# Kernel tuning notes

Hardware: AMD Instinct MI355X
Metric: run time of the kernel (lower is better)

Reference implementation:

```python
import jax, jax.numpy as jnp
import numpy as np

B, N, EPG = 64, 512, 8192
E = B * EPG
K1 = int(np.ceil(0.8 * N))    # 410
K2 = int(np.ceil(0.8 * K1))   # 328


def setup_inputs() -> dict:
    key = jax.random.key(0)
    ks = jax.random.split(key, 32)
    x = jax.random.normal(ks[0], (B * N, 32), jnp.float32)
    edge_attr = jax.random.normal(ks[1], (E, 100), jnp.float32)
    src_l = jax.random.randint(ks[2], (E,), 0, N)
    dst_l = jax.random.randint(ks[3], (E,), 0, N)
    off = jnp.repeat(jnp.arange(B, dtype=jnp.int64) * N, EPG)
    edge_index = jnp.stack([src_l + off, dst_l + off]).astype(jnp.int64)
    batch = jnp.repeat(jnp.arange(B, dtype=jnp.int64), N)

    def lin(k, fin, fout):
        s = 1.0 / np.sqrt(fin)
        k1, k2 = jax.random.split(k)
        return (jax.random.uniform(k1, (fin, fout), jnp.float32, -s, s),
                jax.random.uniform(k2, (fout,), jnp.float32, -s, s))

    dec1_w, dec1_b = lin(ks[4], 100, 64)
    dec2_w, dec2_b = lin(ks[5], 64, 32)
    mlp1_w, mlp1_b = lin(ks[6], 32, 128)
    mlp2_w, mlp2_b = lin(ks[7], 128, 256)
    pool1_w = jax.random.normal(ks[8], (256,), jnp.float32) * 0.1
    gat_w = jax.random.normal(ks[9], (256, 256), jnp.float32) * (1.0 / np.sqrt(256))
    gat_att_src = jax.random.normal(ks[10], (4, 64), jnp.float32) * 0.1
    gat_att_dst = jax.random.normal(ks[11], (4, 64), jnp.float32) * 0.1
    gat_b = jnp.zeros((256,), jnp.float32)
    pool2_w = jax.random.normal(ks[12], (256,), jnp.float32) * 0.1
    lin1_w, lin1_b = lin(ks[13], 512, 128)
    lin2_w, lin2_b = lin(ks[14], 128, 64)
    lin3_w, lin3_b = lin(ks[15], 64, 2)
    return dict(x=x, edge_index=edge_index, batch=batch, edge_attr=edge_attr,
                dec1_w=dec1_w, dec1_b=dec1_b, dec2_w=dec2_w, dec2_b=dec2_b,
                mlp1_w=mlp1_w, mlp1_b=mlp1_b, mlp2_w=mlp2_w, mlp2_b=mlp2_b,
                pool1_w=pool1_w, gat_w=gat_w, gat_att_src=gat_att_src,
                gat_att_dst=gat_att_dst, gat_b=gat_b, pool2_w=pool2_w,
                lin1_w=lin1_w, lin1_b=lin1_b, lin2_w=lin2_w, lin2_b=lin2_b,
                lin3_w=lin3_w, lin3_b=lin3_b)


def _forward(x, edge_attr, dec1_w, dec1_b, dec2_w, dec2_b, mlp1_w, mlp1_b,
             mlp2_w, mlp2_b, pool1_w, gat_w, gat_att_src, gat_att_dst, gat_b,
             pool2_w, lin1_w, lin1_b, lin2_w, lin2_b, lin3_w, lin3_b,
             src, dst):
    # edge encoder
    ea = jax.nn.relu(edge_attr @ dec1_w + dec1_b)
    ea = jax.nn.relu(ea @ dec2_w + dec2_b)                       # [E,32]
    # GINEConv (eps=0): sum_j relu(x_j + e_ji), then mlp((1+eps)x + aggr)
    msg = jax.nn.relu(x[src] + ea)
    agg = jax.ops.segment_sum(msg, dst, num_segments=B * N)
    h = x + agg
    h = jax.nn.relu(h @ mlp1_w + mlp1_b) @ mlp2_w + mlp2_b       # [BN,256]
    h = jax.nn.relu(h)
    # TopKPooling 1 (uniform graphs -> fixed k)
    s = jnp.tanh((h @ pool1_w) / jnp.linalg.norm(pool1_w))       # [BN]
    topv, topi = jax.lax.top_k(s.reshape(B, N), K1)              # [B,K1]
    gperm = (topi + jnp.arange(B)[:, None] * N).reshape(-1)
    hp = h[gperm] * topv.reshape(-1)[:, None]                    # [B*K1,256]
    kept = jnp.zeros(B * N, bool).at[gperm].set(True)
    newid = jnp.zeros(B * N, jnp.int32).at[gperm].set(jnp.arange(B * K1, dtype=jnp.int32))
    src1, dst1 = newid[src], newid[dst]
    valid = kept[src] & kept[dst]
    # readout 1: global max + mean pool
    hr = hp.reshape(B, K1, 256)
    x1 = jnp.concatenate([hr.max(axis=1), hr.mean(axis=1)], axis=-1)  # [B,512]
    # GATConv(256, 64, heads=4) with self-loops; invalid edges masked
    Nk = B * K1
    loops = jnp.arange(Nk, dtype=jnp.int32)
    src2 = jnp.concatenate([src1, loops])
    dst2 = jnp.concatenate([dst1, loops])
    valid2 = jnp.concatenate([valid, jnp.ones(Nk, bool)])
    xl = (hp @ gat_w).reshape(Nk, 4, 64)
    a_src = (xl * gat_att_src).sum(-1)                           # [Nk,4]
    a_dst = (xl * gat_att_dst).sum(-1)
    logit = jax.nn.leaky_relu(a_src[src2] + a_dst[dst2], 0.2)    # [E2,4]
    logit = jnp.where(valid2[:, None], logit, -jnp.inf)
    m = jax.ops.segment_max(logit, dst2, num_segments=Nk)
    e = jnp.where(valid2[:, None], jnp.exp(logit - m[dst2]), 0.0)
    den = jax.ops.segment_sum(e, dst2, num_segments=Nk)
    alpha = e / den[dst2]
    out = jax.ops.segment_sum(alpha[:, :, None] * xl[src2], dst2, num_segments=Nk)
    g = jax.nn.relu(out.reshape(Nk, 256) + gat_b)
    # TopKPooling 2 (pooled edges unused downstream)
    s2 = jnp.tanh((g @ pool2_w) / jnp.linalg.norm(pool2_w))
    topv2, topi2 = jax.lax.top_k(s2.reshape(B, K1), K2)
    gperm2 = (topi2 + jnp.arange(B)[:, None] * K1).reshape(-1)
    gp = (g[gperm2] * topv2.reshape(-1)[:, None]).reshape(B, K2, 256)
    x2 = jnp.concatenate([gp.max(axis=1), gp.mean(axis=1)], axis=-1)
    # head (dropout = identity in eval)
    z = x1 + x2
    z = jax.nn.relu(z @ lin1_w + lin1_b)
    z = jax.nn.relu(z @ lin2_w + lin2_b)
    return jax.nn.log_softmax(z @ lin3_w + lin3_b, axis=-1)     # [B,2]


def reference(x, edge_index, batch, edge_attr, dec1_w, dec1_b, dec2_w, dec2_b,
              mlp1_w, mlp1_b, mlp2_w, mlp2_b, pool1_w, gat_w, gat_att_src,
              gat_att_dst, gat_b, pool2_w, lin1_w, lin1_b, lin2_w, lin2_b,
              lin3_w, lin3_b):
    src = edge_index[0].astype(jnp.int32)
    dst = edge_index[1].astype(jnp.int32)
    return _forward(x, edge_attr, dec1_w, dec1_b, dec2_w, dec2_b, mlp1_w,
                    mlp1_b, mlp2_w, mlp2_b, pool1_w, gat_w, gat_att_src,
                    gat_att_dst, gat_b, pool2_w, lin1_w, lin1_b, lin2_w,
                    lin2_b, lin3_w, lin3_b, src, dst)
```

## Files before the change

### kernel.cpp

```cpp
#include <hip/hip_runtime.h>
#include <math.h>

#define B_   64
#define N_   512
#define E_   524288
#define BN_  32768
#define K1_  410
#define K2_  328
#define NK_  26240
#define KC_  25

__device__ __forceinline__ float lrelu(float x) { return x > 0.f ? x : 0.2f * x; }

__global__ __launch_bounds__(256) void norm_kernel(const float* __restrict__ p1,
                                                   const float* __restrict__ p2,
                                                   float* __restrict__ norms) {
    __shared__ float r1[256], r2[256];
    int t = threadIdx.x;
    float a = p1[t], b = p2[t];
    r1[t] = a * a; r2[t] = b * b;
    for (int o = 128; o > 0; o >>= 1) {
        __syncthreads();
        if (t < o) { r1[t] += r1[t + o]; r2[t] += r2[t + o]; }
    }
    __syncthreads();
    if (t == 0) { norms[0] = sqrtf(r1[0]); norms[1] = sqrtf(r2[0]); }
}

template <int NSEG>
__global__ __launch_bounds__(1024) void scan_kernel(int* __restrict__ cnt, int* __restrict__ offsets)
{
    __shared__ int part[1024];
    int t = threadIdx.x;
    const int CH = (NSEG + 1023) / 1024;
    int base = t * CH;
    int sum = 0;
    for (int i = 0; i < CH; ++i) { int gi = base + i; if (gi < NSEG) sum += cnt[gi]; }
    part[t] = sum;
    __syncthreads();
    for (int o = 1; o < 1024; o <<= 1) {
        int v = (t >= o) ? part[t - o] : 0;
        __syncthreads();
        part[t] += v;
        __syncthreads();
    }
    int run = (t == 0) ? 0 : part[t - 1];
    for (int i = 0; i < CH; ++i) {
        int gi = base + i;
        if (gi < NSEG) { offsets[gi] = run; run += cnt[gi]; cnt[gi] = 0; }
    }
    if (t == 1023) offsets[NSEG] = part[1023];
}

__global__ __launch_bounds__(256) void count_node_kernel(const int* __restrict__ dstG,
                                                         int* __restrict__ cnt_node)
{
    int e = blockIdx.x * blockDim.x + threadIdx.x;
    atomicAdd(&cnt_node[dstG[e]], 1);
}

__global__ __launch_bounds__(256) void fill_node_kernel(const int* __restrict__ dstG,
                                                        const int* __restrict__ offs_node,
                                                        int* __restrict__ cnt_node,
                                                        int* __restrict__ pos_e)
{
    int e = blockIdx.x * blockDim.x + threadIdx.x;
    int d = dstG[e];
    int p = offs_node[d] + atomicAdd(&cnt_node[d], 1);
    pos_e[e] = p;
}

__global__ __launch_bounds__(256) void edge_mlp_kernel(
    const float* __restrict__ edge_attr, const int* __restrict__ srcG,
    const int* __restrict__ pos_e,
    const float* __restrict__ x,
    const float* __restrict__ W1, const float* __restrict__ b1,
    const float* __restrict__ W2, const float* __restrict__ b2,
    float* __restrict__ msg_sorted)
{
    __shared__ float bufAT[KC_][68];
    __shared__ float w1cT[KC_][64];
    __shared__ float ea1T[64][68];
    __shared__ float w2s[64][32];
    __shared__ float b2s[32];
    __shared__ int   srcs[64], poss[64];

    int tid = threadIdx.x;
    int eb  = blockIdx.x * 64;

    if (tid < 64) { srcs[tid] = srcG[eb + tid]; poss[tid] = pos_e[eb + tid]; }
    for (int i = tid; i < 64 * 32; i += 256) w2s[i >> 5][i & 31] = W2[i];
    if (tid >= 192 && tid < 224) b2s[tid - 192] = b2[tid - 192];

    int tx = tid & 15, ty = tid >> 4;
    float b1v[4];
#pragma unroll
    for (int j = 0; j < 4; ++j) b1v[j] = b1[tx * 4 + j];

    float acc[4][4] = {};

    float raA[7], raB[7], rw[7];
    auto issueA = [&](int kc, float (&ra)[7]) {
#pragma unroll
        for (int u = 0; u < 7; ++u) {
            int i = tid + u * 256;
            if (i < 1600) {
                int e = i / 25, k = i - e * 25;
                ra[u] = edge_attr[(size_t)(eb + e) * 100 + kc + k];
            }
        }
    };
    auto issueW = [&](int kc) {
#pragma unroll
        for (int u = 0; u < 7; ++u) {
            int i = tid + u * 256;
            if (i < 1600) rw[u] = W1[(size_t)(kc + (i >> 6)) * 64 + (i & 63)];
        }
    };
    auto lwriteA = [&](float (&ra)[7]) {
#pragma unroll
        for (int u = 0; u < 7; ++u) {
            int i = tid + u * 256;
            if (i < 1600) {
                int e = i / 25, k = i - e * 25;
                bufAT[k][e] = ra[u];
            }
        }
    };
    auto lwriteW = [&]() {
#pragma unroll
        for (int u = 0; u < 7; ++u) {
            int i = tid + u * 256;
            if (i < 1600) w1cT[i >> 6][i & 63] = rw[u];
        }
    };

    issueA(0, raA);
    issueW(0);
    issueA(KC_, raB);
    lwriteA(raA); lwriteW();
    __syncthreads();

#pragma unroll
    for (int c = 0; c < 4; ++c) {
        if (c == 0) issueA(2 * KC_, raA);
        if (c == 1) issueA(3 * KC_, raB);
        if (c < 3)  issueW((c + 1) * KC_);
#pragma unroll 5
        for (int k = 0; k < KC_; ++k) {
            float4 a4 = *(const float4*)&bufAT[k][ty * 4];
            float4 w4 = *(const float4*)&w1cT[k][tx * 4];
            float a[4] = { a4.x, a4.y, a4.z, a4.w };
            float w[4] = { w4.x, w4.y, w4.z, w4.w };
#pragma unroll
            for (int i = 0; i < 4; ++i)
#pragma unroll
                for (int j = 0; j < 4; ++j) acc[i][j] += a[i] * w[j];
        }
        if (c < 3) {
            __syncthreads();
            if ((c & 1) == 0) lwriteA(raB);
            else              lwriteA(raA);
            lwriteW();
            __syncthreads();
        }
    }
#pragma unroll
    for (int j = 0; j < 4; ++j) {
        float4 v;
        v.x = fmaxf(acc[0][j] + b1v[j], 0.f);
        v.y = fmaxf(acc[1][j] + b1v[j], 0.f);
        v.z = fmaxf(acc[2][j] + b1v[j], 0.f);
        v.w = fmaxf(acc[3][j] + b1v[j], 0.f);
        *(float4*)&ea1T[tx * 4 + j][ty * 4] = v;
    }
    __syncthreads();

    int e0 = (tid >> 3) * 2;
    int c0 = (tid & 7) * 4;
    float acc2[2][4] = {};
    for (int k = 0; k < 64; ++k) {
        float2 a2 = *(const float2*)&ea1T[k][e0];
        float4 w4 = *(const float4*)&w2s[k][c0];
        float w[4] = { w4.x, w4.y, w4.z, w4.w };
#pragma unroll
        for (int j = 0; j < 4; ++j) {
            acc2[0][j] += a2.x * w[j]; acc2[1][j] += a2.y * w[j];
        }
    }
#pragma unroll
    for (int r = 0; r < 2; ++r) {
        int e = e0 + r, s = srcs[e];
        const float4 xv = *(const float4*)(x + (size_t)s * 32 + c0);
        float xa[4] = { xv.x, xv.y, xv.z, xv.w };
        float4 m;
        m.x = fmaxf(xa[0] + fmaxf(acc2[r][0] + b2s[c0 + 0], 0.f), 0.f);
        m.y = fmaxf(xa[1] + fmaxf(acc2[r][1] + b2s[c0 + 1], 0.f), 0.f);
        m.z = fmaxf(xa[2] + fmaxf(acc2[r][2] + b2s[c0 + 2], 0.f), 0.f);
        m.w = fmaxf(xa[3] + fmaxf(acc2[r][3] + b2s[c0 + 3], 0.f), 0.f);
        *(float4*)(msg_sorted + (size_t)poss[e] * 32 + c0) = m;
    }
}

__global__ __launch_bounds__(256) void segsum_kernel(const float* __restrict__ msg_sorted,
                                                     const int* __restrict__ offs_n,
                                                     float* __restrict__ agg)
{
    int wid  = (blockIdx.x * blockDim.x + threadIdx.x) >> 6;
    int lane = threadIdx.x & 63;
    if (wid >= BN_) return;
    int off0 = offs_n[wid], off1 = offs_n[wid + 1];
    int col = lane & 31, rr = lane >> 5;
    float sum = 0.f;
    for (int j = off0 + rr; j < off1; j += 2)
        sum += msg_sorted[(size_t)j * 32 + col];
    sum += __shfl_xor(sum, 32);
    if (lane < 32) agg[(size_t)wid * 32 + col] = sum;
}

template <int ACT, bool HASBIAS, bool HASA2, bool GATHER>
__global__ __launch_bounds__(256) void gemm_tile128(
    const float* __restrict__ A, const float* __restrict__ A2,
    const int* __restrict__ rowidx, const float* __restrict__ rowscale,
    const float* __restrict__ W, const float* __restrict__ bias,
    float* __restrict__ C, int M, int N, int K)
{
    __shared__ float As[16][132];
    __shared__ float Ws[16][132];
    int tid = threadIdx.x;
    int tx = tid & 15, ty = tid >> 4;
    int mb = blockIdx.y * 128, nb = blockIdx.x * 128;
    float acc[8][8] = {};

    int am = tid & 127;
    int ak = (tid >> 7) * 8;
    int wk = tid >> 4;
    int wn = (tid & 15) * 8;

    int   arow  = mb + am;
    float ascal = 1.f;
    if (GATHER) { ascal = rowscale[arow]; arow = rowidx[arow]; }

    for (int kt = 0; kt < K; kt += 16) {
        {
            const float* pa = A + (size_t)arow * K + kt + ak;
            float4 v0 = *(const float4*)(pa);
            float4 v1 = *(const float4*)(pa + 4);
            if (HASA2) {
                const float* pb = A2 + (size_t)arow * K + kt + ak;
                float4 u0 = *(const float4*)(pb);
                float4 u1 = *(const float4*)(pb + 4);
                v0.x += u0.x; v0.y += u0.y; v0.z += u0.z; v0.w += u0.w;
                v1.x += u1.x; v1.y += u1.y; v1.z += u1.z; v1.w += u1.w;
            }
            if (GATHER) {
                v0.x *= ascal; v0.y *= ascal; v0.z *= ascal; v0.w *= ascal;
                v1.x *= ascal; v1.y *= ascal; v1.z *= ascal; v1.w *= ascal;
            }
            As[ak + 0][am] = v0.x; As[ak + 1][am] = v0.y;
            As[ak + 2][am] = v0.z; As[ak + 3][am] = v0.w;
            As[ak + 4][am] = v1.x; As[ak + 5][am] = v1.y;
            As[ak + 6][am] = v1.z; As[ak + 7][am] = v1.w;
        }
        {
            const float* pw = W + (size_t)(kt + wk) * N + nb + wn;
            *(float4*)&Ws[wk][wn]     = *(const float4*)(pw);
            *(float4*)&Ws[wk][wn + 4] = *(const float4*)(pw + 4);
        }
        __syncthreads();
#pragma unroll
        for (int k2 = 0; k2 < 16; ++k2) {
            float4 a0 = *(const float4*)&As[k2][ty * 8];
            float4 a1 = *(const float4*)&As[k2][ty * 8 + 4];
            float4 w0 = *(const float4*)&Ws[k2][tx * 4];
            float4 w1 = *(const float4*)&Ws[k2][64 + tx * 4];
            float a[8] = { a0.x, a0.y, a0.z, a0.w, a1.x, a1.y, a1.z, a1.w };
            float w[8] = { w0.x, w0.y, w0.z, w0.w, w1.x, w1.y, w1.z, w1.w };
#pragma unroll
            for (int i = 0; i < 8; ++i)
#pragma unroll
                for (int j = 0; j < 8; ++j) acc[i][j] += a[i] * w[j];
        }
        __syncthreads();
    }
#pragma unroll
    for (int i = 0; i < 8; ++i) {
        int m = mb + ty * 8 + i;
        int col0 = nb + tx * 4, col1 = nb + 64 + tx * 4;
        float r[8];
#pragma unroll
        for (int j = 0; j < 4; ++j) {
            float v = acc[i][j];
            if (HASBIAS) v += bias[col0 + j];
            if (ACT == 1) v = fmaxf(v, 0.f);
            r[j] = v;
        }
#pragma unroll
        for (int j = 4; j < 8; ++j) {
            float v = acc[i][j];
            if (HASBIAS) v += bias[col1 + j - 4];
            if (ACT == 1) v = fmaxf(v, 0.f);
            r[j] = v;
        }
        float4 o0 = { r[0], r[1], r[2], r[3] };
        float4 o1 = { r[4], r[5], r[6], r[7] };
        *(float4*)&C[(size_t)m * N + col0] = o0;
        *(float4*)&C[(size_t)m * N + col1] = o1;
    }
}

__global__ __launch_bounds__(256) void scores_kernel(const float* __restrict__ P,
                                                     const float* __restrict__ w,
                                                     const float* __restrict__ norms, int nidx,
                                                     float* __restrict__ s, int R)
{
    int wid  = (blockIdx.x * blockDim.x + threadIdx.x) >> 6;
    int lane = threadIdx.x & 63;
    if (wid >= R) return;
    float acc = 0.f;
#pragma unroll
    for (int r = 0; r < 4; ++r) {
        int d = r * 64 + lane;
        acc += P[(size_t)wid * 256 + d] * w[d];
    }
    for (int o = 32; o > 0; o >>= 1) acc += __shfl_xor(acc, o);
    if (lane == 0) s[wid] = tanhf(acc / norms[nidx]);
}

__device__ void bitonic_desc512(float* val, int* idx, int t) {
    for (int k = 2; k <= 512; k <<= 1) {
        for (int j = k >> 1; j > 0; j >>= 1) {
            __syncthreads();
            int ixj = t ^ j;
            if (ixj > t) {
                float v0 = val[t], v1 = val[ixj];
                int   i0 = idx[t], i1 = idx[ixj];
                bool before = (v0 > v1) || (v0 == v1 && i0 < i1);
                bool dir = ((t & k) == 0);
                bool doswap = dir ? (!before) : before;
                if (doswap) { val[t] = v1; val[ixj] = v0; idx[t] = i1; idx[ixj] = i0; }
            }
        }
    }
    __syncthreads();
}

__global__ __launch_bounds__(512) void topk1_kernel(const float* __restrict__ s,
                                                    float* __restrict__ topval,
                                                    int* __restrict__ topnode,
                                                    int* __restrict__ kept,
                                                    int* __restrict__ newid)
{
    __shared__ float val[512];
    __shared__ int   idx[512];
    int b = blockIdx.x, t = threadIdx.x;
    val[t] = s[b * N_ + t]; idx[t] = t;
    bitonic_desc512(val, idx, t);
    if (t < K1_) {
        int node = b * N_ + idx[t];
        int orow = b * K1_ + t;
        topnode[orow] = node;
        topval[orow]  = val[t];
        kept[node]  = 1;
        newid[node] = orow;
    }
}

__global__ __launch_bounds__(1024) void readout1_kernel(const float* __restrict__ h,
                                                        const int* __restrict__ topnode,
                                                        const float* __restrict__ topval,
                                                        float* __restrict__ zbuf)
{
    __shared__ float rmx[1024], rsm[1024];
    int b = blockIdx.x >> 2, cg = blockIdx.x & 3;
    int tid = threadIdx.x;
    int cl = tid & 63, rg = tid >> 6;
    int c = cg * 64 + cl;
    float mx = -INFINITY, sm = 0.f;
    for (int j = rg; j < K1_; j += 16) {
        int row = topnode[b * K1_ + j];
        float v = h[(size_t)row * 256 + c] * topval[b * K1_ + j];
        mx = fmaxf(mx, v); sm += v;
    }
    rmx[tid] = mx; rsm[tid] = sm;
    __syncthreads();
    if (tid < 512) { rmx[tid] = fmaxf(rmx[tid], rmx[tid + 512]); rsm[tid] += rsm[tid + 512]; }
    __syncthreads();
    if (tid < 256) { rmx[tid] = fmaxf(rmx[tid], rmx[tid + 256]); rsm[tid] += rsm[tid + 256]; }
    __syncthreads();
    if (tid < 128) { rmx[tid] = fmaxf(rmx[tid], rmx[tid + 128]); rsm[tid] += rsm[tid + 128]; }
    __syncthreads();
    if (tid < 64) {
        zbuf[b * 512 + c]       = fmaxf(rmx[tid], rmx[tid + 64]);
        zbuf[b * 512 + 256 + c] = (rsm[tid] + rsm[tid + 64]) / (float)K1_;
    }
}

__global__ __launch_bounds__(256) void attcoef_kernel(const float* __restrict__ xl,
                                                      const float* __restrict__ att_src,
                                                      const float* __restrict__ att_dst,
                                                      float* __restrict__ a_src,
                                                      float* __restrict__ a_dst)
{
    int wid  = (blockIdx.x * blockDim.x + threadIdx.x) >> 6;
    int lane = threadIdx.x & 63;
    if (wid >= NK_) return;
    float vs[4], vd[4];
#pragma unroll
    for (int r = 0; r < 4; ++r) {
        int d = r * 64 + lane;
        float v = xl[(size_t)wid * 256 + d];
        vs[r] = v * att_src[d];
        vd[r] = v * att_dst[d];
    }
    for (int o = 32; o > 0; o >>= 1) {
#pragma unroll
        for (int r = 0; r < 4; ++r) {
            vs[r] += __shfl_xor(vs[r], o);
            vd[r] += __shfl_xor(vd[r], o);
        }
    }
    if (lane == 0) {
#pragma unroll
        for (int r = 0; r < 4; ++r) {
            a_src[wid * 4 + r] = vs[r];
            a_dst[wid * 4 + r] = vd[r];
        }
    }
}

__global__ __launch_bounds__(256) void count_kernel(const int* __restrict__ srcG,
                                                    const int* __restrict__ dstG,
                                                    const int* __restrict__ kept,
                                                    const int* __restrict__ newid,
                                                    int* __restrict__ cnt)
{
    int e = blockIdx.x * blockDim.x + threadIdx.x;
    int s = srcG[e], d = dstG[e];
    if (kept[s] && kept[d]) atomicAdd(&cnt[newid[d]], 1);
}

__global__ __launch_bounds__(256) void fill_kernel(const int* __restrict__ srcG,
                                                   const int* __restrict__ dstG,
                                                   const int* __restrict__ kept,
                                                   const int* __restrict__ newid,
                                                   const int* __restrict__ offsets,
                                                   int* __restrict__ cnt,
                                                   int* __restrict__ csr_src)
{
    int e = blockIdx.x * blockDim.x + threadIdx.x;
    int s = srcG[e], d = dstG[e];
    if (kept[s] && kept[d]) {
        int d1 = newid[d];
        int p = offsets[d1] + atomicAdd(&cnt[d1], 1);
        csr_src[p] = newid[s];
    }
}

__global__ __launch_bounds__(256) void gat_agg_kernel(const float* __restrict__ xl,
                                                      const float* __restrict__ a_src,
                                                      const float* __restrict__ a_dst,
                                                      const int* __restrict__ offsets,
                                                      const int* __restrict__ csr_src,
                                                      const float* __restrict__ gat_b,
                                                      const float* __restrict__ pool2_w,
                                                      const float* __restrict__ norms,
                                                      float* __restrict__ g,
                                                      float* __restrict__ s2)
{
    int wid  = (blockIdx.x * blockDim.x + threadIdx.x) >> 6;
    int lane = threadIdx.x & 63;
    if (wid >= NK_) return;
    int off0 = offsets[wid], off1 = offsets[wid + 1];

    float4 ad = *(const float4*)(a_dst + (size_t)wid * 4);
    float4 asf = *(const float4*)(a_src + (size_t)wid * 4);
    float adv[4] = { ad.x, ad.y, ad.z, ad.w };
    float lsf[4] = { lrelu(asf.x + ad.x), lrelu(asf.y + ad.y),
                     lrelu(asf.z + ad.z), lrelu(asf.w + ad.w) };

    float den[4] = {};
    float acc[4] = {};
    int e = off0;
    for (; e + 1 < off1; e += 2) {
        int s1 = csr_src[e], s2v = csr_src[e + 1];
        float4 a1 = *(const float4*)(a_src + (size_t)s1 * 4);
        float4 a2 = *(const float4*)(a_src + (size_t)s2v * 4);
        float av1[4] = { a1.x, a1.y, a1.z, a1.w };
        float av2[4] = { a2.x, a2.y, a2.z, a2.w };
#pragma unroll
        for (int r = 0; r < 4; ++r) {
            float w1 = expf(fminf(lrelu(av1[r] + adv[r]), 80.f));
            float w2 = expf(fminf(lrelu(av2[r] + adv[r]), 80.f));
            float x1 = xl[(size_t)s1 * 256 + r * 64 + lane];
            float x2 = xl[(size_t)s2v * 256 + r * 64 + lane];
            den[r] += w1 + w2;
            acc[r] += w1 * x1 + w2 * x2;
        }
    }
    if (e < off1) {
        int s1 = csr_src[e];
        float4 a1 = *(const float4*)(a_src + (size_t)s1 * 4);
        float av1[4] = { a1.x, a1.y, a1.z, a1.w };
#pragma unroll
        for (int r = 0; r < 4; ++r) {
            float w1 = expf(fminf(lrelu(av1[r] + adv[r]), 80.f));
            den[r] += w1;
            acc[r] += w1 * xl[(size_t)s1 * 256 + r * 64 + lane];
        }
    }
    float gv[4];
#pragma unroll
    for (int r = 0; r < 4; ++r) {
        float ws = expf(fminf(lsf[r], 80.f));
        den[r] += ws;
        acc[r] = (acc[r] + ws * xl[(size_t)wid * 256 + r * 64 + lane]) / den[r];
        int d = r * 64 + lane;
        gv[r] = fmaxf(acc[r] + gat_b[d], 0.f);
        g[(size_t)wid * 256 + d] = gv[r];
    }
    float dot = 0.f;
#pragma unroll
    for (int r = 0; r < 4; ++r) dot += gv[r] * pool2_w[r * 64 + lane];
    for (int o = 32; o > 0; o >>= 1) dot += __shfl_xor(dot, o);
    if (lane == 0) s2[wid] = tanhf(dot / norms[1]);
}

__global__ __launch_bounds__(512) void topk2_sort_kernel(const float* __restrict__ s2,
                                                         int* __restrict__ t2row,
                                                         float* __restrict__ t2val)
{
    __shared__ float val[512];
    __shared__ int   idx[512];
    int b = blockIdx.x, t = threadIdx.x;
    val[t] = (t < K1_) ? s2[b * K1_ + t] : -INFINITY;
    idx[t] = t;
    bitonic_desc512(val, idx, t);
    if (t < K2_) {
        t2row[b * K2_ + t] = b * K1_ + idx[t];
        t2val[b * K2_ + t] = val[t];
    }
}

__global__ __launch_bounds__(512) void readout2_kernel(const float* __restrict__ g,
                                                       const int* __restrict__ t2row,
                                                       const float* __restrict__ t2val,
                                                       float* __restrict__ zbuf)
{
    __shared__ float rmx[512], rsm[512];
    int b = blockIdx.x >> 2, cg = blockIdx.x & 3;
    int tid = threadIdx.x;
    int cl = tid & 63, rg = tid >> 6;
    int c = cg * 64 + cl;
    float mx = -INFINITY, sm = 0.f;
    for (int j = rg; j < K2_; j += 8) {
        int row = t2row[b * K2_ + j];
        float v = g[(size_t)row * 256 + c] * t2val[b * K2_ + j];
        mx = fmaxf(mx, v); sm += v;
    }
    rmx[tid] = mx; rsm[tid] = sm;
    __syncthreads();
    if (tid < 256) { rmx[tid] = fmaxf(rmx[tid], rmx[tid + 256]); rsm[tid] += rsm[tid + 256]; }
    __syncthreads();
    if (tid < 128) { rmx[tid] = fmaxf(rmx[tid], rmx[tid + 128]); rsm[tid] += rsm[tid + 128]; }
    __syncthreads();
    if (tid < 64) {
        zbuf[b * 512 + c]       += fmaxf(rmx[tid], rmx[tid + 64]);
        zbuf[b * 512 + 256 + c] += (rsm[tid] + rsm[tid + 64]) / (float)K2_;
    }
}

__global__ __launch_bounds__(128) void head_kernel(const float* __restrict__ zbuf,
                                                   const float* __restrict__ l1w, const float* __restrict__ l1b,
                                                   const float* __restrict__ l2w, const float* __restrict__ l2b,
                                                   const float* __restrict__ l3w, const float* __restrict__ l3b,
                                                   float* __restrict__ out)
{
    __shared__ float zs[512];
    __shared__ float h1s[128];
    __shared__ float h2s[64];
    __shared__ float os[2];
    int b = blockIdx.x, t = threadIdx.x;
    for (int i = t; i < 512; i += 128) zs[i] = zbuf[b * 512 + i];
    __syncthreads();
    float acc = l1b[t];
    for (int k = 0; k < 512; ++k) acc += zs[k] * l1w[k * 128 + t];
    h1s[t] = fmaxf(acc, 0.f);
    __syncthreads();
    if (t < 64) {
        float a2 = l2b[t];
        for (int k = 0; k < 128; ++k) a2 += h1s[k] * l2w[k * 64 + t];
        h2s[t] = fmaxf(a2, 0.f);
    }
    __syncthreads();
    if (t < 2) {
        float a3 = l3b[t];
        for (int k = 0; k < 64; ++k) a3 += h2s[k] * l3w[k * 2 + t];
        os[t] = a3;
    }
    __syncthreads();
    if (t == 0) {
        float m = fmaxf(os[0], os[1]);
        float lse = m + logf(expf(os[0] - m) + expf(os[1] - m));
        out[b * 2 + 0] = os[0] - lse;
        out[b * 2 + 1] = os[1] - lse;
    }
}

extern "C" void kernel_launch(void* const* d_in, const int* in_sizes, int n_in,
                              void* d_out, int out_size, void* d_ws, size_t ws_size,
                              hipStream_t stream)
{
    const float* x         = (const float*)d_in[0];
    const int*   eidx      = (const int*)d_in[1];
    const float* edge_attr = (const float*)d_in[3];
    const float* dec1_w    = (const float*)d_in[4];
    const float* dec1_b    = (const float*)d_in[5];
    const float* dec2_w    = (const float*)d_in[6];
    const float* dec2_b    = (const float*)d_in[7];
    const float* mlp1_w    = (const float*)d_in[8];
    const float* mlp1_b    = (const float*)d_in[9];
    const float* mlp2_w    = (const float*)d_in[10];
    const float* mlp2_b    = (const float*)d_in[11];
    const float* pool1_w   = (const float*)d_in[12];
    const float* gat_w     = (const float*)d_in[13];
    const float* att_src   = (const float*)d_in[14];
    const float* att_dst   = (const float*)d_in[15];
    const float* gat_b     = (const float*)d_in[16];
    const float* pool2_w   = (const float*)d_in[17];
    const float* lin1_w    = (const float*)d_in[18];
    const float* lin1_b    = (const float*)d_in[19];
    const float* lin2_w    = (const float*)d_in[20];
    const float* lin2_b    = (const float*)d_in[21];
    const float* lin3_w    = (const float*)d_in[22];
    const float* lin3_b    = (const float*)d_in[23];
    const int* srcG = eidx;
    const int* dstG = eidx + E_;
    float* out = (float*)d_out;

    char* base = (char*)d_ws;
    size_t o = 0;
    auto alloc = [&](size_t bytes) { size_t r = o; o = (o + bytes + 255) & ~(size_t)255; return r; };
    size_t agg_off    = alloc((size_t)BN_ * 32 * 4);
    size_t cntn_off   = alloc((size_t)BN_ * 4);
    size_t cnt_off    = alloc((size_t)NK_ * 4);
    size_t kept_off   = alloc((size_t)BN_ * 4);
    size_t zero_bytes = o;
    size_t newid_off  = alloc((size_t)BN_ * 4);
    size_t offsn_off  = alloc((size_t)(BN_ + 1) * 4);
    size_t pos_off    = alloc((size_t)E_ * 4);
    size_t h_off      = alloc((size_t)BN_ * 256 * 4);
    size_t hp_off     = alloc((size_t)NK_ * 256 * 4);
    size_t xl_off     = alloc((size_t)NK_ * 256 * 4);
    size_t s_off      = alloc((size_t)BN_ * 4);
    size_t tnode_off  = alloc((size_t)NK_ * 4);
    size_t tval_off   = alloc((size_t)NK_ * 4);
    size_t offs_off   = alloc((size_t)(NK_ + 1) * 4);
    size_t csr_off    = alloc((size_t)E_ * 4);
    size_t zbuf_off   = alloc((size_t)B_ * 512 * 4);
    size_t asrc_off   = alloc((size_t)NK_ * 4 * 4);
    size_t adst_off   = alloc((size_t)NK_ * 4 * 4);
    size_t norm_off   = alloc(256);
    if (o > ws_size) return;

    float* agg      = (float*)(base + agg_off);
    int*   cnt_node = (int*)  (base + cntn_off);
    int*   cnt      = (int*)  (base + cnt_off);
    int*   kept     = (int*)  (base + kept_off);
    int*   newid    = (int*)  (base + newid_off);
    int*   offs_n   = (int*)  (base + offsn_off);
    int*   pos_e    = (int*)  (base + pos_off);
    float* h        = (float*)(base + h_off);
    float* g        = h;
    float* msg      = h;
    float* xl       = (float*)(base + xl_off);
    float* t1       = xl;
    float* s        = (float*)(base + s_off);
    int*   tnode    = (int*)  (base + tnode_off);
    float* tval     = (float*)(base + tval_off);
    int*   offs     = (int*)  (base + offs_off);
    int*   csr      = (int*)  (base + csr_off);
    float* zbuf     = (float*)(base + zbuf_off);
    float* a_src    = (float*)(base + asrc_off);
    float* a_dst    = (float*)(base + adst_off);
    float* norms    = (float*)(base + norm_off);

    hipMemsetAsync(d_ws, 0, zero_bytes, stream);

    norm_kernel<<<1, 256, 0, stream>>>(pool1_w, pool2_w, norms);

    count_node_kernel<<<E_ / 256, 256, 0, stream>>>(dstG, cnt_node);
    scan_kernel<BN_><<<1, 1024, 0, stream>>>(cnt_node, offs_n);
    fill_node_kernel<<<E_ / 256, 256, 0, stream>>>(dstG, offs_n, cnt_node, pos_e);

    edge_mlp_kernel<<<E_ / 64, 256, 0, stream>>>(edge_attr, srcG, pos_e, x,
                                                 dec1_w, dec1_b, dec2_w, dec2_b, msg);
    segsum_kernel<<<BN_ / 4, 256, 0, stream>>>(msg, offs_n, agg);

    gemm_tile128<1, true, true, false><<<dim3(1, BN_ / 128), 256, 0, stream>>>(
        x, agg, nullptr, nullptr, mlp1_w, mlp1_b, t1, BN_, 128, 32);
    gemm_tile128<1, true, false, false><<<dim3(2, BN_ / 128), 256, 0, stream>>>(
        t1, nullptr, nullptr, nullptr, mlp2_w, mlp2_b, h, BN_, 256, 128);

    scores_kernel<<<BN_ / 4, 256, 0, stream>>>(h, pool1_w, norms, 0, s, BN_);
    topk1_kernel<<<B_, 512, 0, stream>>>(s, tval, tnode, kept, newid);
    readout1_kernel<<<B_ * 4, 1024, 0, stream>>>(h, tnode, tval, zbuf);

    gemm_tile128<0, false, false, true><<<dim3(2, NK_ / 128), 256, 0, stream>>>(
        h, nullptr, tnode, tval, gat_w, nullptr, xl, NK_, 256, 256);
    attcoef_kernel<<<NK_ / 4, 256, 0, stream>>>(xl, att_src, att_dst, a_src, a_dst);

    count_kernel<<<E_ / 256, 256, 0, stream>>>(srcG, dstG, kept, newid, cnt);
    scan_kernel<NK_><<<1, 1024, 0, stream>>>(cnt, offs);
    fill_kernel<<<E_ / 256, 256, 0, stream>>>(srcG, dstG, kept, newid, offs, cnt, csr);

    gat_agg_kernel<<<NK_ / 4, 256, 0, stream>>>(xl, a_src, a_dst, offs, csr, gat_b,
                                                pool2_w, norms, g, s);

    topk2_sort_kernel<<<B_, 512, 0, stream>>>(s, tnode, tval);
    readout2_kernel<<<B_ * 4, 512, 0, stream>>>(g, tnode, tval, zbuf);

    head_kernel<<<B_, 128, 0, stream>>>(zbuf, lin1_w, lin1_b, lin2_w, lin2_b,
                                        lin3_w, lin3_b, out);
}
```

Measured before the change: 566.5 us.

## Fuse pool scores and GAT attention coefficients into GEMM epilogues

The score dot-product with pool1_w and the per-head attention coefficients are now computed in the GEMM epilogues. Each thread reduces its partial sums across tx lanes and accumulates them with atomicAdd into zeroed buffers, and a small kernel then applies tanh and the norm. This removes two passes that re-read the 32768x256 and 26240x256 activations, at the cost of extra atomics and shuffles in the GEMM tail. Index arithmetic in the edge-MLP loaders is also precomputed once, outside the repeated issue and LDS-write loops.

```diff
diff --git a/kernel.cpp b/kernel.cpp
--- a/kernel.cpp
+++ b/kernel.cpp
@@ -97,41 +97,44 @@
 #pragma unroll
     for (int j = 0; j < 4; ++j) b1v[j] = b1[tx * 4 + j];
 
+    int attr_base[7], lds_a[7];
+    bool valid[7];
+#pragma unroll
+    for (int u = 0; u < 7; ++u) {
+        int i = tid + u * 256;
+        valid[u] = (i < 1600);
+        int e = i / 25, k = i - e * 25;
+        attr_base[u] = (eb + e) * 100 + k;
+        lds_a[u] = k * 68 + e;
+    }
+    float* bufA0 = &bufAT[0][0];
+    float* w1l   = &w1cT[0][0];
+
     float acc[4][4] = {};
 
     float raA[7], raB[7], rw[7];
     auto issueA = [&](int kc, float (&ra)[7]) {
 #pragma unroll
+        for (int u = 0; u < 7; ++u)
+            if (valid[u]) ra[u] = edge_attr[(size_t)(attr_base[u] + kc)];
+    };
+    auto issueW = [&](int kc) {
+#pragma unroll
         for (int u = 0; u < 7; ++u) {
             int i = tid + u * 256;
-            if (i < 1600) {
-                int e = i / 25, k = i - e * 25;
-                ra[u] = edge_attr[(size_t)(eb + e) * 100 + kc + k];
-            }
+            if (valid[u]) rw[u] = W1[(size_t)kc * 64 + i];
         }
     };
-    auto issueW = [&](int kc) {
+    auto lwriteA = [&](float (&ra)[7]) {
+#pragma unroll
+        for (int u = 0; u < 7; ++u)
+            if (valid[u]) bufA0[lds_a[u]] = ra[u];
+    };
+    auto lwriteW = [&]() {
 #pragma unroll
         for (int u = 0; u < 7; ++u) {
             int i = tid + u * 256;
-            if (i < 1600) rw[u] = W1[(size_t)(kc + (i >> 6)) * 64 + (i & 63)];
-        }
-    };
-    auto lwriteA = [&](float (&ra)[7]) {
-#pragma unroll
-        for (int u = 0; u < 7; ++u) {
-            int i = tid + u * 256;
-            if (i < 1600) {
-                int e = i / 25, k = i - e * 25;
-                bufAT[k][e] = ra[u];
-            }
-        }
-    };
-    auto lwriteW = [&]() {
-#pragma unroll
-        for (int u = 0; u < 7; ++u) {
-            int i = tid + u * 256;
-            if (i < 1600) w1cT[i >> 6][i & 63] = rw[u];
+            if (valid[u]) w1l[i] = rw[u];
         }
     };
 
@@ -218,12 +221,15 @@
     if (lane < 32) agg[(size_t)wid * 32 + col] = sum;
 }
 
-template <int ACT, bool HASBIAS, bool HASA2, bool GATHER>
+template <int ACT, bool HASBIAS, bool HASA2, bool GATHER, bool SCORES, bool ATTC>
 __global__ __launch_bounds__(256) void gemm_tile128(
     const float* __restrict__ A, const float* __restrict__ A2,
     const int* __restrict__ rowidx, const float* __restrict__ rowscale,
     const float* __restrict__ W, const float* __restrict__ bias,
-    float* __restrict__ C, int M, int N, int K)
+    float* __restrict__ C, int M, int N, int K,
+    const float* __restrict__ pvec, float* __restrict__ pout,
+    const float* __restrict__ av_src, const float* __restrict__ av_dst,
+    float* __restrict__ ao_src, float* __restrict__ ao_dst)
 {
     __shared__ float As[16][132];
     __shared__ float Ws[16][132];
@@ -283,10 +289,11 @@
         }
         __syncthreads();
     }
+    int col0 = nb + tx * 4, col1 = nb + 64 + tx * 4;
+    int hd0 = col0 >> 6, hd1 = col1 >> 6;
 #pragma unroll
     for (int i = 0; i < 8; ++i) {
         int m = mb + ty * 8 + i;
-        int col0 = nb + tx * 4, col1 = nb + 64 + tx * 4;
         float r[8];
 #pragma unroll
         for (int j = 0; j < 4; ++j) {
@@ -306,25 +313,47 @@
         float4 o1 = { r[4], r[5], r[6], r[7] };
         *(float4*)&C[(size_t)m * N + col0] = o0;
         *(float4*)&C[(size_t)m * N + col1] = o1;
-    }
-}
-
-__global__ __launch_bounds__(256) void scores_kernel(const float* __restrict__ P,
-                                                     const float* __restrict__ w,
-                                                     const float* __restrict__ norms, int nidx,
-                                                     float* __restrict__ s, int R)
-{
-    int wid  = (blockIdx.x * blockDim.x + threadIdx.x) >> 6;
-    int lane = threadIdx.x & 63;
-    if (wid >= R) return;
-    float acc = 0.f;
-#pragma unroll
-    for (int r = 0; r < 4; ++r) {
-        int d = r * 64 + lane;
-        acc += P[(size_t)wid * 256 + d] * w[d];
-    }
-    for (int o = 32; o > 0; o >>= 1) acc += __shfl_xor(acc, o);
-    if (lane == 0) s[wid] = tanhf(acc / norms[nidx]);
+
+        if (SCORES) {
+            float d = 0.f;
+#pragma unroll
+            for (int j = 0; j < 4; ++j) d += r[j] * pvec[col0 + j];
+#pragma unroll
+            for (int j = 4; j < 8; ++j) d += r[j] * pvec[col1 + j - 4];
+#pragma unroll
+            for (int o = 1; o < 16; o <<= 1) d += __shfl_xor(d, o);
+            if (tx == 0) atomicAdd(&pout[m], d);
+        }
+        if (ATTC) {
+            float sA = 0.f, sB = 0.f, dA = 0.f, dB = 0.f;
+#pragma unroll
+            for (int j = 0; j < 4; ++j) {
+                int w0i = hd0 * 64 + ((col0 & 63) + j);
+                int w1i = hd1 * 64 + ((col1 & 63) + j);
+                sA += r[j] * av_src[w0i];   dA += r[j] * av_dst[w0i];
+                sB += r[j + 4] * av_src[w1i]; dB += r[j + 4] * av_dst[w1i];
+            }
+#pragma unroll
+            for (int o = 1; o < 16; o <<= 1) {
+                sA += __shfl_xor(sA, o); sB += __shfl_xor(sB, o);
+                dA += __shfl_xor(dA, o); dB += __shfl_xor(dB, o);
+            }
+            if (tx == 0) {
+                atomicAdd(&ao_src[m * 4 + hd0], sA);
+                atomicAdd(&ao_src[m * 4 + hd1], sB);
+                atomicAdd(&ao_dst[m * 4 + hd0], dA);
+                atomicAdd(&ao_dst[m * 4 + hd1], dB);
+            }
+        }
+    }
+}
+
+__global__ __launch_bounds__(256) void scores_fin_kernel(float* __restrict__ s,
+                                                         const float* __restrict__ norms,
+                                                         int R)
+{
+    int i = blockIdx.x * blockDim.x + threadIdx.x;
+    if (i < R) s[i] = tanhf(s[i] / norms[0]);
 }
 
 __device__ void bitonic_desc512(float* val, int* idx, int t) {
@@ -393,39 +422,6 @@
     if (tid < 64) {
         zbuf[b * 512 + c]       = fmaxf(rmx[tid], rmx[tid + 64]);
         zbuf[b * 512 + 256 + c] = (rsm[tid] + rsm[tid + 64]) / (float)K1_;
-    }
-}
-
-__global__ __launch_bounds__(256) void attcoef_kernel(const float* __restrict__ xl,
-                                                      const float* __restrict__ att_src,
-                                                      const float* __restrict__ att_dst,
-                                                      float* __restrict__ a_src,
-                                                      float* __restrict__ a_dst)
-{
-    int wid  = (blockIdx.x * blockDim.x + threadIdx.x) >> 6;
-    int lane = threadIdx.x & 63;
-    if (wid >= NK_) return;
-    float vs[4], vd[4];
-#pragma unroll
-    for (int r = 0; r < 4; ++r) {
-        int d = r * 64 + lane;
-        float v = xl[(size_t)wid * 256 + d];
-        vs[r] = v * att_src[d];
-        vd[r] = v * att_dst[d];
-    }
-    for (int o = 32; o > 0; o >>= 1) {
-#pragma unroll
-        for (int r = 0; r < 4; ++r) {
-            vs[r] += __shfl_xor(vs[r], o);
-            vd[r] += __shfl_xor(vd[r], o);
-        }
-    }
-    if (lane == 0) {
-#pragma unroll
-        for (int r = 0; r < 4; ++r) {
-            a_src[wid * 4 + r] = vs[r];
-            a_dst[wid * 4 + r] = vd[r];
-        }
     }
 }
 
@@ -645,6 +641,9 @@
     size_t cntn_off   = alloc((size_t)BN_ * 4);
     size_t cnt_off    = alloc((size_t)NK_ * 4);
     size_t kept_off   = alloc((size_t)BN_ * 4);
+    size_t s_off      = alloc((size_t)BN_ * 4);
+    size_t asrc_off   = alloc((size_t)NK_ * 4 * 4);
+    size_t adst_off   = alloc((size_t)NK_ * 4 * 4);
     size_t zero_bytes = o;
     size_t newid_off  = alloc((size_t)BN_ * 4);
     size_t offsn_off  = alloc((size_t)(BN_ + 1) * 4);
@@ -652,14 +651,11 @@
     size_t h_off      = alloc((size_t)BN_ * 256 * 4);
     size_t hp_off     = alloc((size_t)NK_ * 256 * 4);
     size_t xl_off     = alloc((size_t)NK_ * 256 * 4);
-    size_t s_off      = alloc((size_t)BN_ * 4);
     size_t tnode_off  = alloc((size_t)NK_ * 4);
     size_t tval_off   = alloc((size_t)NK_ * 4);
     size_t offs_off   = alloc((size_t)(NK_ + 1) * 4);
     size_t csr_off    = alloc((size_t)E_ * 4);
     size_t zbuf_off   = alloc((size_t)B_ * 512 * 4);
-    size_t asrc_off   = alloc((size_t)NK_ * 4 * 4);
-    size_t adst_off   = alloc((size_t)NK_ * 4 * 4);
     size_t norm_off   = alloc(256);
     if (o > ws_size) return;
 
@@ -667,6 +663,9 @@
     int*   cnt_node = (int*)  (base + cntn_off);
     int*   cnt      = (int*)  (base + cnt_off);
     int*   kept     = (int*)  (base + kept_off);
+    float* s        = (float*)(base + s_off);
+    float* a_src    = (float*)(base + asrc_off);
+    float* a_dst    = (float*)(base + adst_off);
     int*   newid    = (int*)  (base + newid_off);
     int*   offs_n   = (int*)  (base + offsn_off);
     int*   pos_e    = (int*)  (base + pos_off);
@@ -675,14 +674,11 @@
     float* msg      = h;
     float* xl       = (float*)(base + xl_off);
     float* t1       = xl;
-    float* s        = (float*)(base + s_off);
     int*   tnode    = (int*)  (base + tnode_off);
     float* tval     = (float*)(base + tval_off);
     int*   offs     = (int*)  (base + offs_off);
     int*   csr      = (int*)  (base + csr_off);
     float* zbuf     = (float*)(base + zbuf_off);
-    float* a_src    = (float*)(base + asrc_off);
-    float* a_dst    = (float*)(base + adst_off);
     float* norms    = (float*)(base + norm_off);
 
     hipMemsetAsync(d_ws, 0, zero_bytes, stream);
@@ -697,18 +693,20 @@
                                                  dec1_w, dec1_b, dec2_w, dec2_b, msg);
     segsum_kernel<<<BN_ / 4, 256, 0, stream>>>(msg, offs_n, agg);
 
-    gemm_tile128<1, true, true, false><<<dim3(1, BN_ / 128), 256, 0, stream>>>(
-        x, agg, nullptr, nullptr, mlp1_w, mlp1_b, t1, BN_, 128, 32);
-    gemm_tile128<1, true, false, false><<<dim3(2, BN_ / 128), 256, 0, stream>>>(
-        t1, nullptr, nullptr, nullptr, mlp2_w, mlp2_b, h, BN_, 256, 128);
-
-    scores_kernel<<<BN_ / 4, 256, 0, stream>>>(h, pool1_w, norms, 0, s, BN_);
+    gemm_tile128<1, true, true, false, false, false><<<dim3(1, BN_ / 128), 256, 0, stream>>>(
+        x, agg, nullptr, nullptr, mlp1_w, mlp1_b, t1, BN_, 128, 32,
+        nullptr, nullptr, nullptr, nullptr, nullptr, nullptr);
+    gemm_tile128<1, true, false, false, true, false><<<dim3(2, BN_ / 128), 256, 0, stream>>>(
+        t1, nullptr, nullptr, nullptr, mlp2_w, mlp2_b, h, BN_, 256, 128,
+        pool1_w, s, nullptr, nullptr, nullptr, nullptr);
+
+    scores_fin_kernel<<<BN_ / 256, 256, 0, stream>>>(s, norms, BN_);
     topk1_kernel<<<B_, 512, 0, stream>>>(s, tval, tnode, kept, newid);
     readout1_kernel<<<B_ * 4, 1024, 0, stream>>>(h, tnode, tval, zbuf);
 
-    gemm_tile128<0, false, false, true><<<dim3(2, NK_ / 128), 256, 0, stream>>>(
-        h, nullptr, tnode, tval, gat_w, nullptr, xl, NK_, 256, 256);
-    attcoef_kernel<<<NK_ / 4, 256, 0, stream>>>(xl, att_src, att_dst, a_src, a_dst);
+    gemm_tile128<0, false, false, true, false, true><<<dim3(2, NK_ / 128), 256, 0, stream>>>(
+        h, nullptr, tnode, tval, gat_w, nullptr, xl, NK_, 256, 256,
+        nullptr, nullptr, att_src, att_dst, a_src, a_dst);
 
     count_kernel<<<E_ / 256, 256, 0, stream>>>(srcG, dstG, kept, newid, cnt);
     scan_kernel<NK_><<<1, 1024, 0, stream>>>(cnt, offs);
```

Result: faster. 552.9 us (-2.4%).
